# Kernel optimization log

Measured on AMD Instinct MI355X. Metric: run time of the kernel, lower is better.

## Reference

```python
import jax, jax.numpy as jnp
import numpy as np

N, E, D, H = 50000, 800000, 128, 8
HD = D // H  # 16
HID = 512
EPS = 1e-5
SLOPE = 0.2  # DGL GATConv default negative_slope


def setup_inputs() -> dict:
    key = jax.random.key(0)
    ks = jax.random.split(key, 10)
    s = 0.1
    return {
        "x": jax.random.normal(ks[0], (N, D), jnp.float32),
        "src": jax.random.randint(ks[1], (E,), 0, N),
        "dst": jax.random.randint(ks[2], (E,), 0, N),
        "W": jax.random.normal(ks[3], (D, D), jnp.float32) * s,
        "attn_l": jax.random.normal(ks[4], (H, HD), jnp.float32) * s,
        "attn_r": jax.random.normal(ks[5], (H, HD), jnp.float32) * s,
        "bias_gat": jnp.zeros((D,), jnp.float32),
        "bn1_gamma": jnp.ones((D,), jnp.float32),
        "bn1_beta": jnp.zeros((D,), jnp.float32),
        "W1": jax.random.normal(ks[6], (D, HID), jnp.float32) * s,
        "b1": jnp.zeros((HID,), jnp.float32),
        "W2": jax.random.normal(ks[7], (HID, D), jnp.float32) * s,
        "b2": jnp.zeros((D,), jnp.float32),
        "bn2_gamma": jnp.ones((D,), jnp.float32),
        "bn2_beta": jnp.zeros((D,), jnp.float32),
    }


def _batchnorm(v, gamma, beta):
    # BatchNorm1d, training-mode forward (batch statistics, biased var)
    mu = v.mean(0)
    var = v.var(0)
    return (v - mu) * jax.lax.rsqrt(var + EPS) * gamma + beta


def reference(x, src, dst, W, attn_l, attn_r, bias_gat,
              bn1_gamma, bn1_beta, W1, b1, W2, b2, bn2_gamma, bn2_beta):
    n = x.shape[0]
    # GATConv: project + per-head attention logits
    feat = (x @ W).reshape(n, H, HD)                     # [N, H, hd]
    el = jnp.einsum('nhd,hd->nh', feat, attn_l)          # [N, H]
    er = jnp.einsum('nhd,hd->nh', feat, attn_r)          # [N, H]
    e = el[src] + er[dst]                                # [E, H]
    e = jnp.where(e > 0, e, SLOPE * e)                   # LeakyReLU
    # segment (edge) softmax over incoming edges of each dst node
    m = jax.ops.segment_max(e, dst, num_segments=n)      # [N, H]
    ee = jnp.exp(e - m[dst])
    denom = jax.ops.segment_sum(ee, dst, num_segments=n)
    alpha = ee / denom[dst]                              # [E, H]
    # weighted scatter-aggregate of source features
    msg = feat[src] * alpha[:, :, None]                  # [E, H, hd]
    agg = jax.ops.segment_sum(msg, dst, num_segments=n)  # [N, H, hd]
    h = agg.reshape(n, D) + bias_gat
    # BN -> Linear -> ReLU -> Linear -> BN
    h = _batchnorm(h, bn1_gamma, bn1_beta)
    h = jax.nn.relu(h @ W1 + b1) @ W2 + b2
    h = _batchnorm(h, bn2_gamma, bn2_beta)
    return h
```

## Files before the change

### kernel.cpp

```cpp
#include <hip/hip_runtime.h>
#include <math.h>

#define NHEAD 8
#define DD 128
#define HIDD 512
#define NB 768

typedef _Float16 half8 __attribute__((ext_vector_type(8)));
typedef _Float16 half4 __attribute__((ext_vector_type(4)));
typedef float floatx4 __attribute__((ext_vector_type(4)));

__device__ __forceinline__ int swz256(int row, int bytecol) {
  return row * 256 + (bytecol ^ ((row & 15) << 4));
}
__device__ __forceinline__ int swz512(int row, int bytecol) {
  return row * 512 + (bytecol ^ ((row & 15) << 4));
}

__global__ __launch_bounds__(256) void pack_kernel(
    const float* __restrict__ W, const float* __restrict__ W1,
    const float* __restrict__ W2, _Float16* __restrict__ WP,
    _Float16* __restrict__ W1TP, _Float16* __restrict__ W2P)
{
  int i = blockIdx.x * 256 + threadIdx.x;
  if (i < 4 * 128 * 4 * 8) {
    int ii = i & 7, l4 = (i >> 3) & 3, col = (i >> 5) & 127, kc = i >> 12;
    WP[i] = (_Float16)W[(kc * 32 + l4 * 8 + ii) * DD + col];
  }
  if (i < 65536) {
    int ii = i & 7, e = (i >> 3) & 63, tile = i >> 9;
    int l4 = e >> 4, l15 = e & 15, hb = tile >> 2, kc = tile & 3;
    W1TP[i] = (_Float16)W1[(size_t)(kc * 32 + l4 * 8 + ii) * HIDD + hb * 16 + l15];
  }
  if (i < 65536) {
    int ii = i & 7, e = (i >> 3) & 63, tile = i >> 9;
    int l4 = e >> 4, l15 = e & 15, c = tile >> 3, cb = tile & 7;
    int hidden = (ii < 4) ? (2 * c) * 16 + 4 * l4 + ii
                          : (2 * c + 1) * 16 + 4 * l4 + (ii - 4);
    W2P[i] = (_Float16)W2[(size_t)hidden * DD + cb * 16 + l15];
  }
}

__global__ __launch_bounds__(256) void feat_mfma_kernel(
    const float* __restrict__ x, const _Float16* __restrict__ WP,
    _Float16* __restrict__ feat16, int N, int T)
{
  __shared__ char xs[32 * 512];
  const int tid = threadIdx.x;
  const int wv = tid >> 6, lane = tid & 63;
  const int l15 = lane & 15, l4 = lane >> 4;
  const int row = tid >> 3, seg = tid & 7;

  int t = blockIdx.x;
  float4 pre[4];
  {
    const int n = t * 32 + row;
    const bool ok = (t < T) && (n < N);
    const float4* sp = (const float4*)(x + (size_t)n * DD + seg * 16);
    const float4 z = make_float4(0.f, 0.f, 0.f, 0.f);
    #pragma unroll
    for (int c = 0; c < 4; ++c) pre[c] = ok ? sp[c] : z;
  }

  for (; t < T; t += NB) {
    const int n0 = t * 32;
    #pragma unroll
    for (int c = 0; c < 4; ++c)
      *(float4*)(xs + swz512(row, seg * 64 + c * 16)) = pre[c];
    __syncthreads();

    floatx4 acc[2][2];
    #pragma unroll
    for (int mf = 0; mf < 2; ++mf) { acc[mf][0] = (floatx4)0.f; acc[mf][1] = (floatx4)0.f; }

    #pragma unroll
    for (int kc = 0; kc < 4; ++kc) {
      half8 b0 = *(const half8*)(WP + ((kc * 128 + wv * 32 + l15) * 4 + l4) * 8);
      half8 b1 = *(const half8*)(WP + ((kc * 128 + wv * 32 + 16 + l15) * 4 + l4) * 8);
      #pragma unroll
      for (int mf = 0; mf < 2; ++mf) {
        const int rr = mf * 16 + l15;
        float4 a0 = *(const float4*)(xs + swz512(rr, kc * 128 + l4 * 32));
        float4 a1 = *(const float4*)(xs + swz512(rr, kc * 128 + l4 * 32 + 16));
        half8 af;
        af[0] = (_Float16)a0.x; af[1] = (_Float16)a0.y; af[2] = (_Float16)a0.z; af[3] = (_Float16)a0.w;
        af[4] = (_Float16)a1.x; af[5] = (_Float16)a1.y; af[6] = (_Float16)a1.z; af[7] = (_Float16)a1.w;
        acc[mf][0] = __builtin_amdgcn_mfma_f32_16x16x32_f16(af, b0, acc[mf][0], 0, 0, 0);
        acc[mf][1] = __builtin_amdgcn_mfma_f32_16x16x32_f16(af, b1, acc[mf][1], 0, 0, 0);
      }
    }

    {
      const int tn = t + NB;
      const int n = tn * 32 + row;
      const bool ok = (tn < T) && (n < N);
      const float4* sp = (const float4*)(x + (size_t)n * DD + seg * 16);
      const float4 z = make_float4(0.f, 0.f, 0.f, 0.f);
      #pragma unroll
      for (int c = 0; c < 4; ++c) pre[c] = ok ? sp[c] : z;
    }

    #pragma unroll
    for (int mf = 0; mf < 2; ++mf) {
      #pragma unroll
      for (int r = 0; r < 4; ++r) {
        const int rown = n0 + mf * 16 + l4 * 4 + r;
        if (rown < N) {
          feat16[(size_t)rown * DD + wv * 32 + l15] = (_Float16)acc[mf][0][r];
          feat16[(size_t)rown * DD + wv * 32 + 16 + l15] = (_Float16)acc[mf][1][r];
        }
      }
    }
    __syncthreads();
  }
}

__global__ __launch_bounds__(256) void elr_kernel(
    const _Float16* __restrict__ feat16, const float* __restrict__ attn_l,
    const float* __restrict__ attn_r, float* __restrict__ el,
    float* __restrict__ er, int N)
{
  int gid = blockIdx.x * 256 + threadIdx.x;
  if (gid >= N * NHEAD) return;
  const int n = gid >> 3, h = gid & 7;
  const half8* fp = (const half8*)(feat16 + (size_t)n * DD + h * 16);
  half8 f0 = fp[0], f1 = fp[1];
  float sl = 0.f, sr = 0.f;
  #pragma unroll
  for (int d = 0; d < 8; ++d) {
    float v0 = (float)f0[d], v1 = (float)f1[d];
    sl = fmaf(v0, attn_l[h * 16 + d], sl);
    sl = fmaf(v1, attn_l[h * 16 + 8 + d], sl);
    sr = fmaf(v0, attn_r[h * 16 + d], sr);
    sr = fmaf(v1, attn_r[h * 16 + 8 + d], sr);
  }
  el[gid] = sl;
  er[gid] = sr;
}

__global__ __launch_bounds__(256) void count_kernel(const int* __restrict__ dst,
                                                    int* __restrict__ counts,
                                                    int* __restrict__ rank, int E)
{
  int e = blockIdx.x * 256 + threadIdx.x;
  if (e < E) rank[e] = atomicAdd(&counts[dst[e]], 1);
}

__global__ __launch_bounds__(256) void scan1_kernel(const int* __restrict__ counts,
                                                    int* __restrict__ offsets,
                                                    int* __restrict__ btot)
{
  __shared__ int wsum[4];
  const int lane = threadIdx.x & 63;
  const int wid = threadIdx.x >> 6;
  int4 c = *(const int4*)(counts + blockIdx.x * 1024 + threadIdx.x * 4);
  int q = c.x + c.y + c.z + c.w;
  int incl = q;
  #pragma unroll
  for (int d = 1; d < 64; d <<= 1) {
    int t = __shfl_up(incl, d, 64);
    if (lane >= d) incl += t;
  }
  if (lane == 63) wsum[wid] = incl;
  __syncthreads();
  int wprefix = 0;
  for (int w = 0; w < wid; ++w) wprefix += wsum[w];
  int excl = wprefix + incl - q;
  int4 o;
  o.x = excl; o.y = excl + c.x; o.z = o.y + c.y; o.w = o.z + c.z;
  *(int4*)(offsets + blockIdx.x * 1024 + threadIdx.x * 4) = o;
  if (threadIdx.x == 0) btot[blockIdx.x] = wsum[0] + wsum[1] + wsum[2] + wsum[3];
}

__global__ __launch_bounds__(64) void scan2_kernel(const int* __restrict__ btot,
                                                   int* __restrict__ bof, int nchunk)
{
  const int t = threadIdx.x;
  const int K = (nchunk + 63) >> 6;
  const int base = t * K;
  int s = 0;
  for (int i = 0; i < K; ++i) if (base + i < nchunk) s += btot[base + i];
  int incl = s;
  #pragma unroll
  for (int d = 1; d < 64; d <<= 1) {
    int tt = __shfl_up(incl, d, 64);
    if (t >= d) incl += tt;
  }
  int run = incl - s;
  for (int i = 0; i < K; ++i) if (base + i < nchunk) { bof[base + i] = run; run += btot[base + i]; }
}

__global__ __launch_bounds__(256) void fill_kernel(const int* __restrict__ src,
                                                   const int* __restrict__ dst,
                                                   const int* __restrict__ offsets,
                                                   const int* __restrict__ bof,
                                                   const int* __restrict__ rank,
                                                   int* __restrict__ srcl,
                                                   const float* __restrict__ el,
                                                   const float* __restrict__ er,
                                                   _Float16* __restrict__ p16, int E)
{
  int e = blockIdx.x * 256 + threadIdx.x;
  if (e < E) {
    int s = src[e], d = dst[e];
    int pos = offsets[d] + bof[d >> 10] + rank[e];
    srcl[pos] = s;
    float4 el0 = *(const float4*)(el + (size_t)s * NHEAD);
    float4 el1 = *(const float4*)(el + (size_t)s * NHEAD + 4);
    float4 er0 = *(const float4*)(er + (size_t)d * NHEAD);
    float4 er1 = *(const float4*)(er + (size_t)d * NHEAD + 4);
    float v[8];
    v[0] = el0.x + er0.x; v[1] = el0.y + er0.y; v[2] = el0.z + er0.z; v[3] = el0.w + er0.w;
    v[4] = el1.x + er1.x; v[5] = el1.y + er1.y; v[6] = el1.z + er1.z; v[7] = el1.w + er1.w;
    half8 pv;
    #pragma unroll
    for (int h = 0; h < 8; ++h) {
      float t = v[h] > 0.f ? v[h] : 0.2f * v[h];
      pv[h] = (_Float16)__expf(t);
    }
    *(half8*)(p16 + (size_t)pos * NHEAD) = pv;
  }
}

__global__ __launch_bounds__(256) void agg_kernel(
    const _Float16* __restrict__ feat16, const _Float16* __restrict__ p16,
    const int* __restrict__ offsets, const int* __restrict__ bof,
    const int* __restrict__ srcl, const float* __restrict__ bias,
    float* __restrict__ hout, int N)
{
  int gid = blockIdx.x * 256 + threadIdx.x;
  if (gid >= N * NHEAD) return;
  const int n = gid >> 3, hh = gid & 7;
  const int o0 = offsets[n] + bof[n >> 10];
  const int o1 = offsets[n + 1] + bof[(n + 1) >> 10];

  float s = 0.f;
  float a[16];
  #pragma unroll
  for (int d = 0; d < 16; ++d) a[d] = 0.f;

  int j = o0;
  for (; j + 1 < o1; j += 2) {
    const int s0 = srcl[j], s1 = srcl[j + 1];
    const float pp0 = (float)p16[(size_t)j * NHEAD + hh];
    const float pp1 = (float)p16[(size_t)(j + 1) * NHEAD + hh];
    const half8* f0p = (const half8*)(feat16 + (size_t)s0 * DD + hh * 16);
    const half8* f1p = (const half8*)(feat16 + (size_t)s1 * DD + hh * 16);
    half8 f00 = f0p[0], f01 = f0p[1];
    half8 f10 = f1p[0], f11 = f1p[1];
    s += pp0 + pp1;
    #pragma unroll
    for (int d = 0; d < 8; ++d) {
      a[d]     = fmaf(pp0, (float)f00[d], fmaf(pp1, (float)f10[d], a[d]));
      a[d + 8] = fmaf(pp0, (float)f01[d], fmaf(pp1, (float)f11[d], a[d + 8]));
    }
  }
  if (j < o1) {
    const int s0 = srcl[j];
    const float pp0 = (float)p16[(size_t)j * NHEAD + hh];
    const half8* f0p = (const half8*)(feat16 + (size_t)s0 * DD + hh * 16);
    half8 f00 = f0p[0], f01 = f0p[1];
    s += pp0;
    #pragma unroll
    for (int d = 0; d < 8; ++d) {
      a[d]     = fmaf(pp0, (float)f00[d], a[d]);
      a[d + 8] = fmaf(pp0, (float)f01[d], a[d + 8]);
    }
  }

  const float inv = (o1 > o0) ? 1.f / s : 0.f;
  float* op = hout + (size_t)n * DD + hh * 16;
  const float* bp = bias + hh * 16;
  #pragma unroll
  for (int q = 0; q < 4; ++q) {
    float4 o;
    o.x = fmaf(a[q * 4 + 0], inv, bp[q * 4 + 0]);
    o.y = fmaf(a[q * 4 + 1], inv, bp[q * 4 + 1]);
    o.z = fmaf(a[q * 4 + 2], inv, bp[q * 4 + 2]);
    o.w = fmaf(a[q * 4 + 3], inv, bp[q * 4 + 3]);
    *(float4*)(op + q * 4) = o;
  }
}

__global__ __launch_bounds__(256) void bnstats_kernel(
    const float* __restrict__ h, float* __restrict__ sums,
    float* __restrict__ sumsq, int N)
{
  __shared__ float rs[256], rss[256];
  const int c = threadIdx.x & 127;
  const int half = threadIdx.x >> 7;
  const int rowsPer = (N + gridDim.x - 1) / gridDim.x;
  const int r0 = blockIdx.x * rowsPer;
  const int r1 = min(N, r0 + rowsPer);
  float s = 0.f, ss = 0.f;
  for (int r = r0 + half; r < r1; r += 2) {
    float v = h[(size_t)r * DD + c];
    s += v; ss += v * v;
  }
  rs[threadIdx.x] = s; rss[threadIdx.x] = ss;
  __syncthreads();
  if (threadIdx.x < 128) {
    s = rs[threadIdx.x] + rs[threadIdx.x + 128];
    ss = rss[threadIdx.x] + rss[threadIdx.x + 128];
    atomicAdd(&sums[c], s);
    atomicAdd(&sumsq[c], ss);
  }
}

__global__ __launch_bounds__(64, 2) void mlp_mfma_kernel(
    const float* __restrict__ hbuf, const float* __restrict__ sum1,
    const float* __restrict__ ss1, const float* __restrict__ bn1_g,
    const float* __restrict__ bn1_b, const _Float16* __restrict__ W1TP,
    const _Float16* __restrict__ W2P, const float* __restrict__ b1,
    const float* __restrict__ b2, float* __restrict__ out, int N)
{
  __shared__ char myA[8192];
  const int lane = threadIdx.x;
  const int l15 = lane & 15, l4 = lane >> 4;
  const int n0 = blockIdx.x * 32;
  if (n0 >= N) return;

  const int c0 = (lane & 31) * 4;
  float sc[4], sh[4];
  #pragma unroll
  for (int j = 0; j < 4; ++j) {
    float mean = sum1[c0 + j] / (float)N;
    float var = ss1[c0 + j] / (float)N - mean * mean;
    float s = bn1_g[c0 + j] * rsqrtf(var + 1e-5f);
    sc[j] = s; sh[j] = bn1_b[c0 + j] - mean * s;
  }

  {
    const int rhalf = lane >> 5;
    #pragma unroll
    for (int it = 0; it < 16; ++it) {
      const int row = it * 2 + rhalf;
      const int n = n0 + row;
      float4 v = make_float4(0.f, 0.f, 0.f, 0.f);
      if (n < N) v = *(const float4*)(hbuf + (size_t)n * DD + c0);
      half4 hv;
      hv[0] = (_Float16)fmaf(v.x, sc[0], sh[0]);
      hv[1] = (_Float16)fmaf(v.y, sc[1], sh[1]);
      hv[2] = (_Float16)fmaf(v.z, sc[2], sh[2]);
      hv[3] = (_Float16)fmaf(v.w, sc[3], sh[3]);
      *(half4*)(myA + swz256(row, c0 * 2)) = hv;
    }
  }

  half8 xf[2][4];
  #pragma unroll
  for (int nb = 0; nb < 2; ++nb)
    #pragma unroll
    for (int kc = 0; kc < 4; ++kc)
      xf[nb][kc] = *(const half8*)(myA + swz256(nb * 16 + l15, kc * 64 + l4 * 16));

  floatx4 acc2[2][8];
  #pragma unroll
  for (int nb = 0; nb < 2; ++nb)
    #pragma unroll
    for (int cb = 0; cb < 8; ++cb) acc2[nb][cb] = (floatx4)0.f;

  #pragma unroll
  for (int hp = 0; hp < 2; ++hp) {
    half8 a2s[8][2];
    #pragma unroll
    for (int c8 = 0; c8 < 8; ++c8) {
      const int c = hp * 8 + c8;
      floatx4 dA[2], dB[2];
      dA[0] = (floatx4)0.f; dA[1] = (floatx4)0.f;
      dB[0] = (floatx4)0.f; dB[1] = (floatx4)0.f;
      half8 wA[4], wB[4];
      #pragma unroll
      for (int kc = 0; kc < 4; ++kc) {
        wA[kc] = *(const half8*)(W1TP + (size_t)((2 * c) * 4 + kc) * 512 + (l4 * 16 + l15) * 8);
        wB[kc] = *(const half8*)(W1TP + (size_t)((2 * c + 1) * 4 + kc) * 512 + (l4 * 16 + l15) * 8);
      }
      __builtin_amdgcn_s_setprio(1);
      #pragma unroll
      for (int kc = 0; kc < 4; ++kc) {
        dA[0] = __builtin_amdgcn_mfma_f32_16x16x32_f16(wA[kc], xf[0][kc], dA[0], 0, 0, 0);
        dA[1] = __builtin_amdgcn_mfma_f32_16x16x32_f16(wA[kc], xf[1][kc], dA[1], 0, 0, 0);
        dB[0] = __builtin_amdgcn_mfma_f32_16x16x32_f16(wB[kc], xf[0][kc], dB[0], 0, 0, 0);
        dB[1] = __builtin_amdgcn_mfma_f32_16x16x32_f16(wB[kc], xf[1][kc], dB[1], 0, 0, 0);
      }
      __builtin_amdgcn_s_setprio(0);
      floatx4 bA = *(const floatx4*)&b1[(2 * c) * 16 + l4 * 4];
      floatx4 bB = *(const floatx4*)&b1[(2 * c + 1) * 16 + l4 * 4];
      #pragma unroll
      for (int nb = 0; nb < 2; ++nb) {
        #pragma unroll
        for (int r = 0; r < 4; ++r) {
          float vA = dA[nb][r] + bA[r];
          float vB = dB[nb][r] + bB[r];
          a2s[c8][nb][r]     = (_Float16)(vA > 0.f ? vA : 0.f);
          a2s[c8][nb][r + 4] = (_Float16)(vB > 0.f ? vB : 0.f);
        }
      }
    }
    #pragma unroll
    for (int c8 = 0; c8 < 8; ++c8) {
      const int c = hp * 8 + c8;
      half8 w2[8];
      #pragma unroll
      for (int cb = 0; cb < 8; ++cb)
        w2[cb] = *(const half8*)(W2P + (size_t)(c * 8 + cb) * 512 + (l4 * 16 + l15) * 8);
      __builtin_amdgcn_s_setprio(1);
      #pragma unroll
      for (int cb = 0; cb < 8; ++cb) {
        acc2[0][cb] = __builtin_amdgcn_mfma_f32_16x16x32_f16(a2s[c8][0], w2[cb], acc2[0][cb], 0, 0, 0);
        acc2[1][cb] = __builtin_amdgcn_mfma_f32_16x16x32_f16(a2s[c8][1], w2[cb], acc2[1][cb], 0, 0, 0);
      }
      __builtin_amdgcn_s_setprio(0);
    }
  }

  float b2v[8];
  #pragma unroll
  for (int cb = 0; cb < 8; ++cb) b2v[cb] = b2[cb * 16 + l15];
  #pragma unroll
  for (int nb = 0; nb < 2; ++nb) {
    #pragma unroll
    for (int r = 0; r < 4; ++r) {
      const int rown = n0 + nb * 16 + l4 * 4 + r;
      if (rown < N) {
        #pragma unroll
        for (int cb = 0; cb < 8; ++cb)
          out[(size_t)rown * DD + cb * 16 + l15] = acc2[nb][cb][r] + b2v[cb];
      }
    }
  }
}

__global__ __launch_bounds__(256) void applybn_kernel(
    float* __restrict__ out, const float* __restrict__ sum2,
    const float* __restrict__ ss2, const float* __restrict__ gamma,
    const float* __restrict__ beta, int N, int total4)
{
  __shared__ float sc[128], sh[128];
  if (threadIdx.x < 128) {
    int c = threadIdx.x;
    float mean = sum2[c] / (float)N;
    float var = ss2[c] / (float)N - mean * mean;
    float s = gamma[c] * rsqrtf(var + 1e-5f);
    sc[c] = s;
    sh[c] = beta[c] - mean * s;
  }
  __syncthreads();
  int i = blockIdx.x * 256 + threadIdx.x;
  const int stride = gridDim.x * 256;
  for (; i < total4; i += stride) {
    float4 v = ((float4*)out)[i];
    int c = (i & 31) * 4;
    float4 scv = *(const float4*)&sc[c];
    float4 shv = *(const float4*)&sh[c];
    v.x = fmaf(v.x, scv.x, shv.x); v.y = fmaf(v.y, scv.y, shv.y);
    v.z = fmaf(v.z, scv.z, shv.z); v.w = fmaf(v.w, scv.w, shv.w);
    ((float4*)out)[i] = v;
  }
}

extern "C" void kernel_launch(void* const* d_in, const int* in_sizes, int n_in,
                              void* d_out, int out_size, void* d_ws, size_t ws_size,
                              hipStream_t stream) {
  const float* x        = (const float*)d_in[0];
  const int*   src      = (const int*)d_in[1];
  const int*   dst      = (const int*)d_in[2];
  const float* W        = (const float*)d_in[3];
  const float* attn_l   = (const float*)d_in[4];
  const float* attn_r   = (const float*)d_in[5];
  const float* bias_gat = (const float*)d_in[6];
  const float* bn1_g    = (const float*)d_in[7];
  const float* bn1_b    = (const float*)d_in[8];
  const float* W1       = (const float*)d_in[9];
  const float* b1       = (const float*)d_in[10];
  const float* W2       = (const float*)d_in[11];
  const float* b2       = (const float*)d_in[12];
  const float* bn2_g    = (const float*)d_in[13];
  const float* bn2_b    = (const float*)d_in[14];
  float* out = (float*)d_out;

  const int N = in_sizes[0] / DD;
  const int E = in_sizes[1];
  const int NPAD = ((N + 1023) / 1024) * 1024;
  const int NCHUNK = NPAD / 1024;
  const int T = (N + 31) / 32;

  _Float16* feat16 = (_Float16*)d_ws;
  float* hbuf = (float*)(feat16 + (size_t)((N + 1) & ~1) * DD);
  float* el   = hbuf + (size_t)N * DD;
  float* er   = el + (size_t)N * NHEAD;
  int* counts = (int*)(er + (size_t)N * NHEAD);
  int* offsets = counts + NPAD;
  int* srcl   = offsets + NPAD;
  _Float16* p16 = (_Float16*)(srcl + E);
  int* btot   = (int*)(p16 + (size_t)E * NHEAD);
  int* bof    = btot + 64;
  float* stats = (float*)(bof + 64);
  float* sum1 = stats, *ss1 = stats + 128;
  float* sum2 = stats + 256, *ss2 = stats + 384;
  _Float16* WP   = (_Float16*)(stats + 1024);
  _Float16* W1TP = WP + 4 * 128 * 32;
  _Float16* W2P  = W1TP + 65536;
  int* rank = (int*)hbuf;

  hipMemsetAsync(counts, 0, (size_t)NPAD * sizeof(int), stream);
  hipMemsetAsync(stats, 0, 512 * sizeof(float), stream);

  pack_kernel<<<256, 256, 0, stream>>>(W, W1, W2, WP, W1TP, W2P);
  feat_mfma_kernel<<<NB, 256, 0, stream>>>(x, WP, feat16, N, T);
  elr_kernel<<<(N * NHEAD + 255) / 256, 256, 0, stream>>>(feat16, attn_l, attn_r, el, er, N);
  count_kernel<<<(E + 255) / 256, 256, 0, stream>>>(dst, counts, rank, E);
  scan1_kernel<<<NCHUNK, 256, 0, stream>>>(counts, offsets, btot);
  scan2_kernel<<<1, 64, 0, stream>>>(btot, bof, NCHUNK);
  fill_kernel<<<(E + 255) / 256, 256, 0, stream>>>(src, dst, offsets, bof, rank, srcl,
                                                   el, er, p16, E);
  agg_kernel<<<(N * NHEAD + 255) / 256, 256, 0, stream>>>(feat16, p16, offsets, bof,
                                                          srcl, bias_gat, hbuf, N);
  bnstats_kernel<<<256, 256, 0, stream>>>(hbuf, sum1, ss1, N);
  mlp_mfma_kernel<<<T, 64, 0, stream>>>(hbuf, sum1, ss1, bn1_g, bn1_b, W1TP, W2P,
                                        b1, b2, out, N);
  bnstats_kernel<<<256, 256, 0, stream>>>(out, sum2, ss2, N);
  applybn_kernel<<<2048, 256, 0, stream>>>(out, sum2, ss2, bn2_g, bn2_b, N, N * DD / 4);
}
```

Measured before the change: 250.1 us.

## Split GAT aggregation edges across thread pairs and MLP hidden dim across two waves

The aggregation kernel now gives each (node, head) two threads, each summing half of the incoming edges. Partial sums are combined with a lane shuffle, and each thread writes half of the 16 output columns. The MLP kernel goes from one wave to two waves per 32-row tile, with each wave handling half of the 512 hidden units. The second-layer partial accumulators are exchanged through shared memory and added by wave 0. Both changes aim at more parallelism and latency hiding, at the cost of extra shuffles, a shared-memory exchange, and fp16 rounding of one partial sum.

```diff
diff --git a/kernel.cpp b/kernel.cpp
--- a/kernel.cpp
+++ b/kernel.cpp
@@ -229,18 +229,24 @@
     float* __restrict__ hout, int N)
 {
   int gid = blockIdx.x * 256 + threadIdx.x;
-  if (gid >= N * NHEAD) return;
-  const int n = gid >> 3, hh = gid & 7;
+  if (gid >= N * 16) return;
+  const int n = gid >> 4;
+  const int sub = gid & 15;
+  const int hh = sub >> 1;
+  const int half = sub & 1;
   const int o0 = offsets[n] + bof[n >> 10];
   const int o1 = offsets[n + 1] + bof[(n + 1) >> 10];
+  const int cnt = o1 - o0;
+  const int mid = o0 + ((cnt + 1) >> 1);
+  int j = half ? mid : o0;
+  const int je = half ? o1 : mid;
 
   float s = 0.f;
   float a[16];
   #pragma unroll
   for (int d = 0; d < 16; ++d) a[d] = 0.f;
 
-  int j = o0;
-  for (; j + 1 < o1; j += 2) {
+  for (; j + 1 < je; j += 2) {
     const int s0 = srcl[j], s1 = srcl[j + 1];
     const float pp0 = (float)p16[(size_t)j * NHEAD + hh];
     const float pp1 = (float)p16[(size_t)(j + 1) * NHEAD + hh];
@@ -255,7 +261,7 @@
       a[d + 8] = fmaf(pp0, (float)f01[d], fmaf(pp1, (float)f11[d], a[d + 8]));
     }
   }
-  if (j < o1) {
+  if (j < je) {
     const int s0 = srcl[j];
     const float pp0 = (float)p16[(size_t)j * NHEAD + hh];
     const half8* f0p = (const half8*)(feat16 + (size_t)s0 * DD + hh * 16);
@@ -268,18 +274,26 @@
     }
   }
 
-  const float inv = (o1 > o0) ? 1.f / s : 0.f;
-  float* op = hout + (size_t)n * DD + hh * 16;
-  const float* bp = bias + hh * 16;
-  #pragma unroll
-  for (int q = 0; q < 4; ++q) {
-    float4 o;
-    o.x = fmaf(a[q * 4 + 0], inv, bp[q * 4 + 0]);
-    o.y = fmaf(a[q * 4 + 1], inv, bp[q * 4 + 1]);
-    o.z = fmaf(a[q * 4 + 2], inv, bp[q * 4 + 2]);
-    o.w = fmaf(a[q * 4 + 3], inv, bp[q * 4 + 3]);
-    *(float4*)(op + q * 4) = o;
-  }
+  s += __shfl_xor(s, 1, 64);
+  #pragma unroll
+  for (int d = 0; d < 16; ++d) a[d] += __shfl_xor(a[d], 1, 64);
+
+  const float inv = (cnt > 0) ? 1.f / s : 0.f;
+  const int cbase = hh * 16 + half * 8;
+  float* op = hout + (size_t)n * DD + cbase;
+  const float* bp = bias + cbase;
+  const int abase = half * 8;
+  float4 o0v, o1v;
+  o0v.x = fmaf(a[abase + 0], inv, bp[0]);
+  o0v.y = fmaf(a[abase + 1], inv, bp[1]);
+  o0v.z = fmaf(a[abase + 2], inv, bp[2]);
+  o0v.w = fmaf(a[abase + 3], inv, bp[3]);
+  o1v.x = fmaf(a[abase + 4], inv, bp[4]);
+  o1v.y = fmaf(a[abase + 5], inv, bp[5]);
+  o1v.z = fmaf(a[abase + 6], inv, bp[6]);
+  o1v.w = fmaf(a[abase + 7], inv, bp[7]);
+  *(float4*)(op) = o0v;
+  *(float4*)(op + 4) = o1v;
 }
 
 __global__ __launch_bounds__(256) void bnstats_kernel(
@@ -307,7 +321,7 @@
   }
 }
 
-__global__ __launch_bounds__(64, 2) void mlp_mfma_kernel(
+__global__ __launch_bounds__(128, 2) void mlp_mfma_kernel(
     const float* __restrict__ hbuf, const float* __restrict__ sum1,
     const float* __restrict__ ss1, const float* __restrict__ bn1_g,
     const float* __restrict__ bn1_b, const _Float16* __restrict__ W1TP,
@@ -315,26 +329,28 @@
     const float* __restrict__ b2, float* __restrict__ out, int N)
 {
   __shared__ char myA[8192];
-  const int lane = threadIdx.x;
+  __shared__ char xch[8192];
+  const int tid = threadIdx.x;
+  const int wv = tid >> 6;
+  const int lane = tid & 63;
   const int l15 = lane & 15, l4 = lane >> 4;
   const int n0 = blockIdx.x * 32;
   if (n0 >= N) return;
 
-  const int c0 = (lane & 31) * 4;
-  float sc[4], sh[4];
-  #pragma unroll
-  for (int j = 0; j < 4; ++j) {
-    float mean = sum1[c0 + j] / (float)N;
-    float var = ss1[c0 + j] / (float)N - mean * mean;
-    float s = bn1_g[c0 + j] * rsqrtf(var + 1e-5f);
-    sc[j] = s; sh[j] = bn1_b[c0 + j] - mean * s;
-  }
-
   {
-    const int rhalf = lane >> 5;
-    #pragma unroll
-    for (int it = 0; it < 16; ++it) {
-      const int row = it * 2 + rhalf;
+    const int c0 = (tid & 31) * 4;
+    const int rq = tid >> 5;
+    float sc[4], sh[4];
+    #pragma unroll
+    for (int jj = 0; jj < 4; ++jj) {
+      float mean = sum1[c0 + jj] / (float)N;
+      float var = ss1[c0 + jj] / (float)N - mean * mean;
+      float s = bn1_g[c0 + jj] * rsqrtf(var + 1e-5f);
+      sc[jj] = s; sh[jj] = bn1_b[c0 + jj] - mean * s;
+    }
+    #pragma unroll
+    for (int it = 0; it < 8; ++it) {
+      const int row = it * 4 + rq;
       const int n = n0 + row;
       float4 v = make_float4(0.f, 0.f, 0.f, 0.f);
       if (n < N) v = *(const float4*)(hbuf + (size_t)n * DD + c0);
@@ -346,6 +362,7 @@
       *(half4*)(myA + swz256(row, c0 * 2)) = hv;
     }
   }
+  __syncthreads();
 
   half8 xf[2][4];
   #pragma unroll
@@ -360,72 +377,93 @@
     #pragma unroll
     for (int cb = 0; cb < 8; ++cb) acc2[nb][cb] = (floatx4)0.f;
 
-  #pragma unroll
-  for (int hp = 0; hp < 2; ++hp) {
-    half8 a2s[8][2];
-    #pragma unroll
-    for (int c8 = 0; c8 < 8; ++c8) {
-      const int c = hp * 8 + c8;
-      floatx4 dA[2], dB[2];
-      dA[0] = (floatx4)0.f; dA[1] = (floatx4)0.f;
-      dB[0] = (floatx4)0.f; dB[1] = (floatx4)0.f;
-      half8 wA[4], wB[4];
-      #pragma unroll
-      for (int kc = 0; kc < 4; ++kc) {
-        wA[kc] = *(const half8*)(W1TP + (size_t)((2 * c) * 4 + kc) * 512 + (l4 * 16 + l15) * 8);
-        wB[kc] = *(const half8*)(W1TP + (size_t)((2 * c + 1) * 4 + kc) * 512 + (l4 * 16 + l15) * 8);
+  half8 a2s[8][2];
+  #pragma unroll
+  for (int c8 = 0; c8 < 8; ++c8) {
+    const int c = wv * 8 + c8;
+    floatx4 dA[2], dB[2];
+    dA[0] = (floatx4)0.f; dA[1] = (floatx4)0.f;
+    dB[0] = (floatx4)0.f; dB[1] = (floatx4)0.f;
+    half8 wA[4], wB[4];
+    #pragma unroll
+    for (int kc = 0; kc < 4; ++kc) {
+      wA[kc] = *(const half8*)(W1TP + (size_t)((2 * c) * 4 + kc) * 512 + (l4 * 16 + l15) * 8);
+      wB[kc] = *(const half8*)(W1TP + (size_t)((2 * c + 1) * 4 + kc) * 512 + (l4 * 16 + l15) * 8);
+    }
+    __builtin_amdgcn_s_setprio(1);
+    #pragma unroll
+    for (int kc = 0; kc < 4; ++kc) {
+      dA[0] = __builtin_amdgcn_mfma_f32_16x16x32_f16(wA[kc], xf[0][kc], dA[0], 0, 0, 0);
+      dA[1] = __builtin_amdgcn_mfma_f32_16x16x32_f16(wA[kc], xf[1][kc], dA[1], 0, 0, 0);
+      dB[0] = __builtin_amdgcn_mfma_f32_16x16x32_f16(wB[kc], xf[0][kc], dB[0], 0, 0, 0);
+      dB[1] = __builtin_amdgcn_mfma_f32_16x16x32_f16(wB[kc], xf[1][kc], dB[1], 0, 0, 0);
+    }
+    __builtin_amdgcn_s_setprio(0);
+    floatx4 bA = *(const floatx4*)&b1[(2 * c) * 16 + l4 * 4];
+    floatx4 bB = *(const floatx4*)&b1[(2 * c + 1) * 16 + l4 * 4];
+    #pragma unroll
+    for (int nb = 0; nb < 2; ++nb) {
+      #pragma unroll
+      for (int r = 0; r < 4; ++r) {
+        float vA = dA[nb][r] + bA[r];
+        float vB = dB[nb][r] + bB[r];
+        a2s[c8][nb][r]     = (_Float16)(vA > 0.f ? vA : 0.f);
+        a2s[c8][nb][r + 4] = (_Float16)(vB > 0.f ? vB : 0.f);
       }
-      __builtin_amdgcn_s_setprio(1);
-      #pragma unroll
-      for (int kc = 0; kc < 4; ++kc) {
-        dA[0] = __builtin_amdgcn_mfma_f32_16x16x32_f16(wA[kc], xf[0][kc], dA[0], 0, 0, 0);
-        dA[1] = __builtin_amdgcn_mfma_f32_16x16x32_f16(wA[kc], xf[1][kc], dA[1], 0, 0, 0);
-        dB[0] = __builtin_amdgcn_mfma_f32_16x16x32_f16(wB[kc], xf[0][kc], dB[0], 0, 0, 0);
-        dB[1] = __builtin_amdgcn_mfma_f32_16x16x32_f16(wB[kc], xf[1][kc], dB[1], 0, 0, 0);
+    }
+  }
+  #pragma unroll
+  for (int c8 = 0; c8 < 8; ++c8) {
+    const int c = wv * 8 + c8;
+    half8 w2[8];
+    #pragma unroll
+    for (int cb = 0; cb < 8; ++cb)
+      w2[cb] = *(const half8*)(W2P + (size_t)(c * 8 + cb) * 512 + (l4 * 16 + l15) * 8);
+    __builtin_amdgcn_s_setprio(1);
+    #pragma unroll
+    for (int cb = 0; cb < 8; ++cb) {
+      acc2[0][cb] = __builtin_amdgcn_mfma_f32_16x16x32_f16(a2s[c8][0], w2[cb], acc2[0][cb], 0, 0, 0);
+      acc2[1][cb] = __builtin_amdgcn_mfma_f32_16x16x32_f16(a2s[c8][1], w2[cb], acc2[1][cb], 0, 0, 0);
+    }
+    __builtin_amdgcn_s_setprio(0);
+  }
+
+  if (wv == 1) {
+    #pragma unroll
+    for (int nb = 0; nb < 2; ++nb) {
+      #pragma unroll
+      for (int cb = 0; cb < 8; ++cb) {
+        half4 hv;
+        #pragma unroll
+        for (int r = 0; r < 4; ++r) hv[r] = (_Float16)acc2[nb][cb][r];
+        *(half4*)(xch + ((nb * 8 + cb) * 64 + lane) * 8) = hv;
       }
-      __builtin_amdgcn_s_setprio(0);
-      floatx4 bA = *(const floatx4*)&b1[(2 * c) * 16 + l4 * 4];
-      floatx4 bB = *(const floatx4*)&b1[(2 * c + 1) * 16 + l4 * 4];
-      #pragma unroll
-      for (int nb = 0; nb < 2; ++nb) {
+    }
+  }
+  __syncthreads();
+  if (wv == 0) {
+    float b2v[8];
+    #pragma unroll
+    for (int cb = 0; cb < 8; ++cb) b2v[cb] = b2[cb * 16 + l15];
+    #pragma unroll
+    for (int nb = 0; nb < 2; ++nb) {
+      #pragma unroll
+      for (int cb = 0; cb < 8; ++cb) {
+        half4 hv = *(const half4*)(xch + ((nb * 8 + cb) * 64 + lane) * 8);
         #pragma unroll
-        for (int r = 0; r < 4; ++r) {
-          float vA = dA[nb][r] + bA[r];
-          float vB = dB[nb][r] + bB[r];
-          a2s[c8][nb][r]     = (_Float16)(vA > 0.f ? vA : 0.f);
-          a2s[c8][nb][r + 4] = (_Float16)(vB > 0.f ? vB : 0.f);
+        for (int r = 0; r < 4; ++r) acc2[nb][cb][r] += (float)hv[r];
+      }
+    }
+    #pragma unroll
+    for (int nb = 0; nb < 2; ++nb) {
+      #pragma unroll
+      for (int r = 0; r < 4; ++r) {
+        const int rown = n0 + nb * 16 + l4 * 4 + r;
+        if (rown < N) {
+          #pragma unroll
+          for (int cb = 0; cb < 8; ++cb)
+            out[(size_t)rown * DD + cb * 16 + l15] = acc2[nb][cb][r] + b2v[cb];
         }
-      }
-    }
-    #pragma unroll
-    for (int c8 = 0; c8 < 8; ++c8) {
-      const int c = hp * 8 + c8;
-      half8 w2[8];
-      #pragma unroll
-      for (int cb = 0; cb < 8; ++cb)
-        w2[cb] = *(const half8*)(W2P + (size_t)(c * 8 + cb) * 512 + (l4 * 16 + l15) * 8);
-      __builtin_amdgcn_s_setprio(1);
-      #pragma unroll
-      for (int cb = 0; cb < 8; ++cb) {
-        acc2[0][cb] = __builtin_amdgcn_mfma_f32_16x16x32_f16(a2s[c8][0], w2[cb], acc2[0][cb], 0, 0, 0);
-        acc2[1][cb] = __builtin_amdgcn_mfma_f32_16x16x32_f16(a2s[c8][1], w2[cb], acc2[1][cb], 0, 0, 0);
-      }
-      __builtin_amdgcn_s_setprio(0);
-    }
-  }
-
-  float b2v[8];
-  #pragma unroll
-  for (int cb = 0; cb < 8; ++cb) b2v[cb] = b2[cb * 16 + l15];
-  #pragma unroll
-  for (int nb = 0; nb < 2; ++nb) {
-    #pragma unroll
-    for (int r = 0; r < 4; ++r) {
-      const int rown = n0 + nb * 16 + l4 * 4 + r;
-      if (rown < N) {
-        #pragma unroll
-        for (int cb = 0; cb < 8; ++cb)
-          out[(size_t)rown * DD + cb * 16 + l15] = acc2[nb][cb][r] + b2v[cb];
       }
     }
   }
@@ -514,11 +552,11 @@
   scan2_kernel<<<1, 64, 0, stream>>>(btot, bof, NCHUNK);
   fill_kernel<<<(E + 255) / 256, 256, 0, stream>>>(src, dst, offsets, bof, rank, srcl,
                                                    el, er, p16, E);
-  agg_kernel<<<(N * NHEAD + 255) / 256, 256, 0, stream>>>(feat16, p16, offsets, bof,
-                                                          srcl, bias_gat, hbuf, N);
+  agg_kernel<<<(N * 16 + 255) / 256, 256, 0, stream>>>(feat16, p16, offsets, bof,
+                                                       srcl, bias_gat, hbuf, N);
   bnstats_kernel<<<256, 256, 0, stream>>>(hbuf, sum1, ss1, N);
-  mlp_mfma_kernel<<<T, 64, 0, stream>>>(hbuf, sum1, ss1, bn1_g, bn1_b, W1TP, W2P,
-                                        b1, b2, out, N);
+  mlp_mfma_kernel<<<T, 128, 0, stream>>>(hbuf, sum1, ss1, bn1_g, bn1_b, W1TP, W2P,
+                                         b1, b2, out, N);
   bnstats_kernel<<<256, 256, 0, stream>>>(out, sum2, ss2, N);
   applybn_kernel<<<2048, 256, 0, stream>>>(out, sum2, ss2, bn2_g, bn2_b, N, N * DD / 4);
 }
```

After: 249.4 us. Within noise of the previous version (-0.3%).
